# Performance work log

Measured on AMD Instinct MI355X. Metric: run time of the kernel, lower is better.

The kernel has to match this reference:

```python
import jax, jax.numpy as jnp
import numpy as np

SIGMA = 5.0
KSIZE = 31  # int(6*sigma+1), odd
CHANNEL = 3

def build_gaussian_kernel(size, sigma):
    coords = jnp.arange(size, dtype=jnp.float32) - size // 2
    g = jnp.exp(-coords ** 2 / (2.0 * sigma ** 2))
    g = g / g.sum()
    k2d = g[:, None] * g[None, :]            # (k, k)
    # depthwise kernel: (O=C, I/g=1, k, k)
    return jnp.broadcast_to(k2d[None, None], (CHANNEL, 1, size, size))

def depthwise_blur(x, kernel):
    # x: (B, C, H, W); kernel: (C, 1, k, k); groups = C, SAME-style padding k//2
    pad = KSIZE // 2
    return jax.lax.conv_general_dilated(
        x, kernel,
        window_strides=(1, 1),
        padding=((pad, pad), (pad, pad)),
        dimension_numbers=("NCHW", "OIHW", "NCHW"),
        feature_group_count=CHANNEL,
    )

def setup_inputs() -> dict:
    key = jax.random.key(0)
    k1, k2 = jax.random.split(key)
    B, C, H, W = 16, 3, 512, 512
    background = jax.random.uniform(k1, (B, C, H, W), dtype=jnp.float32)
    insatance = jax.random.uniform(k2, (B, C, H, W), dtype=jnp.float32)
    gaussian_kernel = build_gaussian_kernel(KSIZE, SIGMA)
    return {"background": background, "insatance": insatance,
            "gaussian_kernel": gaussian_kernel}

def reference(background, insatance, gaussian_kernel):
    # retinex_decompose(background): only illumination1 is used downstream
    bg_log = jnp.log1p(background)
    illumination1 = depthwise_blur(bg_log, gaussian_kernel)
    # retinex_decompose(insatance): reflectance2 = log1p(ins) - blur(log1p(ins))
    ins_log = jnp.log1p(insatance)
    illumination2 = depthwise_blur(ins_log, gaussian_kernel)
    reflectance2 = ins_log - illumination2
    # adjust_illumination(reflectance2, illumination1)
    img_log = reflectance2 + illumination1
    img_corrected = jnp.clip(jnp.expm1(img_log), 0.0, 1.0)
    return img_corrected
```

## Files before the change

kernel.cpp:

```cpp
#include <hip/hip_runtime.h>


constexpr int W_ = 512, H_ = 512, NIMG = 48;
constexpr int SPITCH = 100;
constexpr int RPITCH = 68;

typedef float v2f __attribute__((ext_vector_type(2)));

#define LDS_BARRIER()                                      \
  do {                                                     \
    asm volatile("" ::: "memory");                         \
    asm volatile("s_waitcnt lgkmcnt(0)" ::: "memory");     \
    __builtin_amdgcn_s_barrier();                          \
    asm volatile("" ::: "memory");                         \
  } while (0)

__device__ constexpr float G[31] = {
    8.8805851e-04f, 1.5861066e-03f, 2.7217699e-03f, 4.4874399e-03f,
    7.1084368e-03f, 1.0818767e-02f, 1.5820117e-02f, 2.2226435e-02f,
    3.0002549e-02f, 3.8911209e-02f, 4.8486352e-02f, 5.8048702e-02f,
    6.6771901e-02f, 7.3794364e-02f, 7.8357552e-02f, 7.9940480e-02f,
    7.8357552e-02f, 7.3794364e-02f, 6.6771901e-02f, 5.8048702e-02f,
    4.8486352e-02f, 3.8911209e-02f, 3.0002549e-02f, 2.2226435e-02f,
    1.5820117e-02f, 1.0818767e-02f, 7.1084368e-03f, 4.4874399e-03f,
    2.7217699e-03f, 1.5861066e-03f, 8.8805851e-04f};

__device__ constexpr float gc(int c) { return (c >= 0 && c < 31) ? G[c] : 0.f; }

__global__ __launch_bounds__(256, 3) void retinex_roll(const float* __restrict__ bg,
                                                       const float* __restrict__ ins,
                                                       float* __restrict__ out) {
  __shared__ __align__(16) float sd[32 * SPITCH];
  __shared__ __align__(16) float hr[64 * RPITCH];

  const int tid  = threadIdx.x;
  const int lane = tid & 63;
  const int x0 = blockIdx.x * 64;
  const int y0 = blockIdx.y * 256;
  const size_t base = (size_t)blockIdx.z * (size_t)(H_ * W_);

  int sr[3], sc[3], gx[3]; bool okx[3];
#pragma unroll
  for (int s = 0; s < 3; ++s) {
    const int item = tid + 256 * s;
    sr[s] = item / 24;
    sc[s] = item - 24 * sr[s];
    gx[s] = x0 - 16 + 4 * sc[s];
    okx[s] = (unsigned)gx[s] < (unsigned)W_;
  }
  const int hrow = tid >> 3;
  const int hcg  = tid & 7;
  const int eg = __builtin_amdgcn_readfirstlane(tid >> 6);

  float4 pb[3], pn[3];
#pragma unroll
  for (int s = 0; s < 3; ++s) {
    const int gy = y0 - 15 + sr[s];
    pb[s] = make_float4(0.f, 0.f, 0.f, 0.f);
    pn[s] = pb[s];
    if (okx[s] && (unsigned)gy < (unsigned)H_) {
      const size_t a = base + (size_t)gy * W_ + gx[s];
      pb[s] = *(const float4*)(bg + a);
      pn[s] = *(const float4*)(ins + a);
    }
  }

#pragma unroll 1
  for (int k = 0; k < 9; ++k) {
#pragma unroll
    for (int s = 0; s < 3; ++s) {
      float4 v;
      v.x = __builtin_amdgcn_logf(1.f + pb[s].x) - __builtin_amdgcn_logf(1.f + pn[s].x);
      v.y = __builtin_amdgcn_logf(1.f + pb[s].y) - __builtin_amdgcn_logf(1.f + pn[s].y);
      v.z = __builtin_amdgcn_logf(1.f + pb[s].z) - __builtin_amdgcn_logf(1.f + pn[s].z);
      v.w = __builtin_amdgcn_logf(1.f + pb[s].w) - __builtin_amdgcn_logf(1.f + pn[s].w);
      *(float4*)(sd + sr[s] * SPITCH + 4 * sc[s]) = v;
    }
    if (k < 8) {
#pragma unroll
      for (int s = 0; s < 3; ++s) {
        const int gy = y0 + 32 * (k + 1) - 15 + sr[s];
        float4 b0 = make_float4(0.f, 0.f, 0.f, 0.f), n0 = b0;
        if (okx[s] && (unsigned)gy < (unsigned)H_) {
          const size_t a = base + (size_t)gy * W_ + gx[s];
          b0 = *(const float4*)(bg + a);
          n0 = *(const float4*)(ins + a);
        }
        pb[s] = b0; pn[s] = n0;
      }
    }
    LDS_BARRIER();

    {
      v2f o2[4];
#pragma unroll
      for (int m = 0; m < 4; ++m) o2[m] = (v2f){0.f, 0.f};
      const float4* p4 = (const float4*)(sd + hrow * SPITCH) + 2 * hcg;
#pragma unroll
      for (int q = 0; q < 10; ++q) {
        const float4 v = p4[q];
        const float w[4] = {v.x, v.y, v.z, v.w};
#pragma unroll
        for (int t = 0; t < 4; ++t) {
          const int pos = 4 * q + t;
          const v2f vv = {w[t], w[t]};
#pragma unroll
          for (int m = 0; m < 4; ++m) {
            const int c0 = pos - 1 - 2 * m;
            if (c0 >= 0 && c0 < 32) {
              const v2f kc = {gc(c0), gc(c0 - 1)};
              o2[m] = __builtin_elementwise_fma(vv, kc, o2[m]);
            }
          }
        }
      }
      const int slot = (32 * k - 15 + hrow + 128) & 63;
      float* dst = hr + slot * RPITCH + 8 * hcg;
      *(float4*)(dst)     = make_float4(o2[0].x, o2[0].y, o2[1].x, o2[1].y);
      *(float4*)(dst + 4) = make_float4(o2[2].x, o2[2].y, o2[3].x, o2[3].y);
    }
    LDS_BARRIER();

    if (k >= 1) {
      const int t0 = 32 * (k - 1) + 8 * eg;
      float insv[8];
#pragma unroll
      for (int p = 0; p < 8; ++p)
        insv[p] = ins[base + (size_t)(y0 + t0 + p) * W_ + x0 + lane];
      v2f acc2[4];
#pragma unroll
      for (int m = 0; m < 4; ++m) acc2[m] = (v2f){0.f, 0.f};
#pragma unroll
      for (int j = 0; j < 38; ++j) {
        const int row = (t0 - 15 + j + 128) & 63;
        const float v = hr[row * RPITCH + lane];
        const v2f vv = {v, v};
#pragma unroll
        for (int m = 0; m < 4; ++m) {
          const int c0 = j - 2 * m;
          if (c0 >= 0 && c0 < 32) {
            const v2f kc = {gc(c0), gc(c0 - 1)};
            acc2[m] = __builtin_elementwise_fma(vv, kc, acc2[m]);
          }
        }
      }
#pragma unroll
      for (int p = 0; p < 8; ++p) {
        const float a = (p & 1) ? acc2[p >> 1].y : acc2[p >> 1].x;
        const size_t ga = base + (size_t)(y0 + t0 + p) * W_ + x0 + lane;
        float r = (1.f + insv[p]) * __builtin_amdgcn_exp2f(a) - 1.f;
        out[ga] = fminf(fmaxf(r, 0.f), 1.f);
      }
    }
  }
}

extern "C" void kernel_launch(void* const* d_in, const int* in_sizes, int n_in,
                              void* d_out, int out_size, void* d_ws, size_t ws_size,
                              hipStream_t stream) {
  const float* bg  = (const float*)d_in[0];
  const float* ins = (const float*)d_in[1];
  float* out = (float*)d_out;
  retinex_roll<<<dim3(8, 2, NIMG), dim3(256), 0, stream>>>(bg, ins, out);
}
```

Baseline: 151.9 us.

## Warp-specialize horizontal and vertical blur passes with a deeper row ring

```diff
diff --git a/kernel.cpp b/kernel.cpp
--- a/kernel.cpp
+++ b/kernel.cpp
@@ -4,16 +4,9 @@
 constexpr int W_ = 512, H_ = 512, NIMG = 48;
 constexpr int SPITCH = 100;
 constexpr int RPITCH = 68;
+constexpr int RSLOTS = 96;
 
 typedef float v2f __attribute__((ext_vector_type(2)));
-
-#define LDS_BARRIER()                                      \
-  do {                                                     \
-    asm volatile("" ::: "memory");                         \
-    asm volatile("s_waitcnt lgkmcnt(0)" ::: "memory");     \
-    __builtin_amdgcn_s_barrier();                          \
-    asm volatile("" ::: "memory");                         \
-  } while (0)
 
 __device__ constexpr float G[31] = {
     8.8805851e-04f, 1.5861066e-03f, 2.7217699e-03f, 4.4874399e-03f,
@@ -31,10 +24,9 @@
                                                        const float* __restrict__ ins,
                                                        float* __restrict__ out) {
   __shared__ __align__(16) float sd[32 * SPITCH];
-  __shared__ __align__(16) float hr[64 * RPITCH];
+  __shared__ __align__(16) float hr[RSLOTS * RPITCH];
 
   const int tid  = threadIdx.x;
-  const int lane = tid & 63;
   const int x0 = blockIdx.x * 64;
   const int y0 = blockIdx.y * 256;
   const size_t base = (size_t)blockIdx.z * (size_t)(H_ * W_);
@@ -48,9 +40,12 @@
     gx[s] = x0 - 16 + 4 * sc[s];
     okx[s] = (unsigned)gx[s] < (unsigned)W_;
   }
-  const int hrow = tid >> 3;
-  const int hcg  = tid & 7;
-  const int eg = __builtin_amdgcn_readfirstlane(tid >> 6);
+  const bool is_h = (tid < 128);
+  const int hrow = tid >> 2;
+  const int hc16 = tid & 3;
+  const int et    = tid & 127;
+  const int elane = et & 63;
+  const int eg = __builtin_amdgcn_readfirstlane(et >> 6);
 
   float4 pb[3], pn[3];
 #pragma unroll
@@ -66,17 +61,19 @@
   }
 
 #pragma unroll 1
-  for (int k = 0; k < 9; ++k) {
+  for (int k = 0; k < 10; ++k) {
+    if (k <= 8) {
 #pragma unroll
-    for (int s = 0; s < 3; ++s) {
-      float4 v;
-      v.x = __builtin_amdgcn_logf(1.f + pb[s].x) - __builtin_amdgcn_logf(1.f + pn[s].x);
-      v.y = __builtin_amdgcn_logf(1.f + pb[s].y) - __builtin_amdgcn_logf(1.f + pn[s].y);
-      v.z = __builtin_amdgcn_logf(1.f + pb[s].z) - __builtin_amdgcn_logf(1.f + pn[s].z);
-      v.w = __builtin_amdgcn_logf(1.f + pb[s].w) - __builtin_amdgcn_logf(1.f + pn[s].w);
-      *(float4*)(sd + sr[s] * SPITCH + 4 * sc[s]) = v;
+      for (int s = 0; s < 3; ++s) {
+        float4 v;
+        v.x = __builtin_amdgcn_logf(1.f + pb[s].x) - __builtin_amdgcn_logf(1.f + pn[s].x);
+        v.y = __builtin_amdgcn_logf(1.f + pb[s].y) - __builtin_amdgcn_logf(1.f + pn[s].y);
+        v.z = __builtin_amdgcn_logf(1.f + pb[s].z) - __builtin_amdgcn_logf(1.f + pn[s].z);
+        v.w = __builtin_amdgcn_logf(1.f + pb[s].w) - __builtin_amdgcn_logf(1.f + pn[s].w);
+        *(float4*)(sd + sr[s] * SPITCH + 4 * sc[s]) = v;
+      }
     }
-    if (k < 8) {
+    if (k <= 7) {
 #pragma unroll
       for (int s = 0; s < 3; ++s) {
         const int gy = y0 + 32 * (k + 1) - 15 + sr[s];
@@ -89,54 +86,61 @@
         pb[s] = b0; pn[s] = n0;
       }
     }
-    LDS_BARRIER();
+    __syncthreads();
 
-    {
-      v2f o2[4];
+    if (is_h) {
+      if (k <= 8) {
+        v2f o2[8];
 #pragma unroll
-      for (int m = 0; m < 4; ++m) o2[m] = (v2f){0.f, 0.f};
-      const float4* p4 = (const float4*)(sd + hrow * SPITCH) + 2 * hcg;
+        for (int m = 0; m < 8; ++m) o2[m] = (v2f){0.f, 0.f};
+        const float4* p4 = (const float4*)(sd + hrow * SPITCH) + hc16 * 4;
 #pragma unroll
-      for (int q = 0; q < 10; ++q) {
-        const float4 v = p4[q];
-        const float w[4] = {v.x, v.y, v.z, v.w};
+        for (int q = 0; q < 12; ++q) {
+          const float4 v = p4[q];
+          const float w4[4] = {v.x, v.y, v.z, v.w};
 #pragma unroll
-        for (int t = 0; t < 4; ++t) {
-          const int pos = 4 * q + t;
-          const v2f vv = {w[t], w[t]};
+          for (int t = 0; t < 4; ++t) {
+            const int w = 4 * q + t;
+            const v2f vv = {w4[t], w4[t]};
 #pragma unroll
-          for (int m = 0; m < 4; ++m) {
-            const int c0 = pos - 1 - 2 * m;
-            if (c0 >= 0 && c0 < 32) {
-              const v2f kc = {gc(c0), gc(c0 - 1)};
-              o2[m] = __builtin_elementwise_fma(vv, kc, o2[m]);
+            for (int m = 0; m < 8; ++m) {
+              const int c0 = w - 1 - 2 * m;
+              if (c0 >= 0 && c0 < 32) {
+                const v2f kc = {gc(c0), gc(c0 - 1)};
+                o2[m] = __builtin_elementwise_fma(vv, kc, o2[m]);
+              }
             }
           }
         }
+        int u = 32 * k + 81 + hrow;
+        u -= (u >= 192) ? 192 : 0;
+        u -= (u >= 96) ? 96 : 0;
+        float* dst = hr + u * RPITCH + 16 * hc16;
+        *(float4*)(dst +  0) = make_float4(o2[0].x, o2[0].y, o2[1].x, o2[1].y);
+        *(float4*)(dst +  4) = make_float4(o2[2].x, o2[2].y, o2[3].x, o2[3].y);
+        *(float4*)(dst +  8) = make_float4(o2[4].x, o2[4].y, o2[5].x, o2[5].y);
+        *(float4*)(dst + 12) = make_float4(o2[6].x, o2[6].y, o2[7].x, o2[7].y);
       }
-      const int slot = (32 * k - 15 + hrow + 128) & 63;
-      float* dst = hr + slot * RPITCH + 8 * hcg;
-      *(float4*)(dst)     = make_float4(o2[0].x, o2[0].y, o2[1].x, o2[1].y);
-      *(float4*)(dst + 4) = make_float4(o2[2].x, o2[2].y, o2[3].x, o2[3].y);
-    }
-    LDS_BARRIER();
-
-    if (k >= 1) {
-      const int t0 = 32 * (k - 1) + 8 * eg;
-      float insv[8];
+    } else if (k >= 2) {
+      const int t0 = 32 * (k - 2) + 16 * eg;
+      int eb = t0 + 81;
+      eb -= (eb >= 192) ? 192 : 0;
+      eb -= (eb >= 96) ? 96 : 0;
+      float insv[16];
 #pragma unroll
-      for (int p = 0; p < 8; ++p)
-        insv[p] = ins[base + (size_t)(y0 + t0 + p) * W_ + x0 + lane];
-      v2f acc2[4];
+      for (int p = 0; p < 16; ++p)
+        insv[p] = ins[base + (size_t)(y0 + t0 + p) * W_ + x0 + elane];
+      v2f acc2[8];
 #pragma unroll
-      for (int m = 0; m < 4; ++m) acc2[m] = (v2f){0.f, 0.f};
+      for (int m = 0; m < 8; ++m) acc2[m] = (v2f){0.f, 0.f};
 #pragma unroll
-      for (int j = 0; j < 38; ++j) {
-        const int row = (t0 - 15 + j + 128) & 63;
-        const float v = hr[row * RPITCH + lane];
+      for (int j = 0; j < 46; ++j) {
+        int row = eb + j;
+        row -= (row >= 96) ? 96 : 0;
+        const float v = hr[row * RPITCH + elane];
         const v2f vv = {v, v};
 #pragma unroll
-        for (int m = 0; m < 4; ++m) {
+        for (int m = 0; m < 8; ++m) {
           const int c0 = j - 2 * m;
           if (c0 >= 0 && c0 < 32) {
             const v2f kc = {gc(c0), gc(c0 - 1)};
@@ -145,13 +149,14 @@
         }
       }
 #pragma unroll
-      for (int p = 0; p < 8; ++p) {
+      for (int p = 0; p < 16; ++p) {
         const float a = (p & 1) ? acc2[p >> 1].y : acc2[p >> 1].x;
-        const size_t ga = base + (size_t)(y0 + t0 + p) * W_ + x0 + lane;
+        const size_t ga = base + (size_t)(y0 + t0 + p) * W_ + x0 + elane;
         float r = (1.f + insv[p]) * __builtin_amdgcn_exp2f(a) - 1.f;
         out[ga] = fminf(fmaxf(r, 0.f), 1.f);
       }
     }
+    __syncthreads();
   }
 }
 
```

Result: slower. 155.1 us (+2.1%).

## Skew horizontal and vertical passes by one stage with a deeper row ring buffer

Applied to the files above, without the earlier changes.

```diff
diff --git a/kernel.cpp b/kernel.cpp
--- a/kernel.cpp
+++ b/kernel.cpp
@@ -4,16 +4,9 @@
 constexpr int W_ = 512, H_ = 512, NIMG = 48;
 constexpr int SPITCH = 100;
 constexpr int RPITCH = 68;
+constexpr int RSLOTS = 96;
 
 typedef float v2f __attribute__((ext_vector_type(2)));
-
-#define LDS_BARRIER()                                      \
-  do {                                                     \
-    asm volatile("" ::: "memory");                         \
-    asm volatile("s_waitcnt lgkmcnt(0)" ::: "memory");     \
-    __builtin_amdgcn_s_barrier();                          \
-    asm volatile("" ::: "memory");                         \
-  } while (0)
 
 __device__ constexpr float G[31] = {
     8.8805851e-04f, 1.5861066e-03f, 2.7217699e-03f, 4.4874399e-03f,
@@ -31,7 +24,7 @@
                                                        const float* __restrict__ ins,
                                                        float* __restrict__ out) {
   __shared__ __align__(16) float sd[32 * SPITCH];
-  __shared__ __align__(16) float hr[64 * RPITCH];
+  __shared__ __align__(16) float hr[RSLOTS * RPITCH];
 
   const int tid  = threadIdx.x;
   const int lane = tid & 63;
@@ -66,17 +59,19 @@
   }
 
 #pragma unroll 1
-  for (int k = 0; k < 9; ++k) {
+  for (int k = 0; k < 10; ++k) {
+    if (k <= 8) {
 #pragma unroll
-    for (int s = 0; s < 3; ++s) {
-      float4 v;
-      v.x = __builtin_amdgcn_logf(1.f + pb[s].x) - __builtin_amdgcn_logf(1.f + pn[s].x);
-      v.y = __builtin_amdgcn_logf(1.f + pb[s].y) - __builtin_amdgcn_logf(1.f + pn[s].y);
-      v.z = __builtin_amdgcn_logf(1.f + pb[s].z) - __builtin_amdgcn_logf(1.f + pn[s].z);
-      v.w = __builtin_amdgcn_logf(1.f + pb[s].w) - __builtin_amdgcn_logf(1.f + pn[s].w);
-      *(float4*)(sd + sr[s] * SPITCH + 4 * sc[s]) = v;
+      for (int s = 0; s < 3; ++s) {
+        float4 v;
+        v.x = __builtin_amdgcn_logf(1.f + pb[s].x) - __builtin_amdgcn_logf(1.f + pn[s].x);
+        v.y = __builtin_amdgcn_logf(1.f + pb[s].y) - __builtin_amdgcn_logf(1.f + pn[s].y);
+        v.z = __builtin_amdgcn_logf(1.f + pb[s].z) - __builtin_amdgcn_logf(1.f + pn[s].z);
+        v.w = __builtin_amdgcn_logf(1.f + pb[s].w) - __builtin_amdgcn_logf(1.f + pn[s].w);
+        *(float4*)(sd + sr[s] * SPITCH + 4 * sc[s]) = v;
+      }
     }
-    if (k < 8) {
+    if (k <= 7) {
 #pragma unroll
       for (int s = 0; s < 3; ++s) {
         const int gy = y0 + 32 * (k + 1) - 15 + sr[s];
@@ -89,9 +84,9 @@
         pb[s] = b0; pn[s] = n0;
       }
     }
-    LDS_BARRIER();
+    __syncthreads();
 
-    {
+    if (k <= 8) {
       v2f o2[4];
 #pragma unroll
       for (int m = 0; m < 4; ++m) o2[m] = (v2f){0.f, 0.f};
@@ -99,11 +94,11 @@
 #pragma unroll
       for (int q = 0; q < 10; ++q) {
         const float4 v = p4[q];
-        const float w[4] = {v.x, v.y, v.z, v.w};
+        const float w4[4] = {v.x, v.y, v.z, v.w};
 #pragma unroll
         for (int t = 0; t < 4; ++t) {
           const int pos = 4 * q + t;
-          const v2f vv = {w[t], w[t]};
+          const v2f vv = {w4[t], w4[t]};
 #pragma unroll
           for (int m = 0; m < 4; ++m) {
             const int c0 = pos - 1 - 2 * m;
@@ -114,15 +109,18 @@
           }
         }
       }
-      const int slot = (32 * k - 15 + hrow + 128) & 63;
-      float* dst = hr + slot * RPITCH + 8 * hcg;
+      int u = 32 * k + 81 + hrow;
+      u -= (u >= 192) ? 192 : 0;
+      u -= (u >= 96) ? 96 : 0;
+      float* dst = hr + u * RPITCH + 8 * hcg;
       *(float4*)(dst)     = make_float4(o2[0].x, o2[0].y, o2[1].x, o2[1].y);
       *(float4*)(dst + 4) = make_float4(o2[2].x, o2[2].y, o2[3].x, o2[3].y);
     }
-    LDS_BARRIER();
-
-    if (k >= 1) {
-      const int t0 = 32 * (k - 1) + 8 * eg;
+    if (k >= 2) {
+      const int t0 = 32 * (k - 2) + 8 * eg;
+      int eb = t0 + 81;
+      eb -= (eb >= 192) ? 192 : 0;
+      eb -= (eb >= 96) ? 96 : 0;
       float insv[8];
 #pragma unroll
       for (int p = 0; p < 8; ++p)
@@ -132,7 +130,8 @@
       for (int m = 0; m < 4; ++m) acc2[m] = (v2f){0.f, 0.f};
 #pragma unroll
       for (int j = 0; j < 38; ++j) {
-        const int row = (t0 - 15 + j + 128) & 63;
+        int row = eb + j;
+        row -= (row >= 96) ? 96 : 0;
         const float v = hr[row * RPITCH + lane];
         const v2f vv = {v, v};
 #pragma unroll
@@ -152,6 +151,7 @@
         out[ga] = fminf(fmaxf(r, 0.f), 1.f);
       }
     }
+    __syncthreads();
   }
 }
 
```

Result: no change. 154.1 us (+1.5%).
